# Kernel optimization log

Measured on AMD Instinct MI355X. Metric: run time of the kernel, lower is better.

Reference implementation:

```python
import jax, jax.numpy as jnp
import numpy as np

REG_MAX = 16  # number of DFL bins per box side
N = 1_048_576  # number of box predictions


def setup_inputs() -> dict:
    key = jax.random.key(0)
    k1, k2, k3 = jax.random.split(key, 3)
    pred = jax.random.normal(k1, (N, 4 * REG_MAX), dtype=jnp.float32)
    # targets are continuous bin coordinates in [0, reg_max - 1]
    target = jax.random.uniform(k2, (N, 4), dtype=jnp.float32, minval=0.0, maxval=REG_MAX - 1)
    weight = jax.random.uniform(k3, (N, 1), dtype=jnp.float32)
    return {"pred": pred, "target": target, "weight": weight}


def _target_distribution(target):
    # two-hot soft label: mass split between floor(t) and floor(t)+1 bins
    t = jnp.clip(target, 0.0, REG_MAX - 1)              # [N,4]
    left = jnp.floor(t).astype(jnp.int32)               # [N,4]
    right = jnp.clip(left + 1, 0, REG_MAX - 1)          # [N,4]
    w_right = t - left.astype(t.dtype)
    w_left = 1.0 - w_right
    oh_left = jax.nn.one_hot(left, REG_MAX, dtype=t.dtype)   # [N,4,REG_MAX]
    oh_right = jax.nn.one_hot(right, REG_MAX, dtype=t.dtype)
    return oh_left * w_left[..., None] + oh_right * w_right[..., None]


def reference(pred, target, weight):
    p = pred.reshape(-1, 4, REG_MAX)                     # [N,4,REG_MAX]
    td = _target_distribution(target.reshape(-1, 4))     # [N,4,REG_MAX]
    logp = jax.nn.log_softmax(p, axis=-1)
    # KL-div pointwise: td * (log(td) - logp), with 0 where td == 0 (xlogy semantics)
    safe_log_td = jnp.log(jnp.where(td > 0, td, 1.0))
    kl = jnp.where(td > 0, td * (safe_log_td - logp), 0.0).sum(axis=-1)  # [N,4]
    loss = kl * weight                                    # weight broadcasts [N,1] -> [N,4]
    return loss.mean()
```

## Files before the change

### kernel.cpp

```cpp
#include <hip/hip_runtime.h>

#define REG_MAX 16
#define NROWS   1048576
#define NTASK   (NROWS * 4)
#define NBLOCKS 2048
#define NTHREADS 256

__device__ __forceinline__ float dfl_task(const float* __restrict__ pred,
                                          const float* __restrict__ target,
                                          const float* __restrict__ weight,
                                          int task, int q)
{
    const float4 v = *reinterpret_cast<const float4*>(
        pred + (size_t)task * REG_MAX + q * 4);

    float s = __expf(v.x) + __expf(v.y) + __expf(v.z) + __expf(v.w);
    s += __shfl_xor(s, 1);
    s += __shfl_xor(s, 2);
    const float lse = __logf(s);

    float t = target[task];
    t = fminf(fmaxf(t, 0.0f), 15.0f);
    const float lf = floorf(t);
    const int   li = (int)lf;
    const int   ri = min(li + 1, REG_MAX - 1);
    const float wr = t - lf;
    const float wl = 1.0f - wr;

    float kl = 0.0f;
    const int base = q * 4;

    {
        const int il = li - base;
        if (il >= 0 && il < 4) {
            float pv = v.x;
            pv = (il == 1) ? v.y : pv;
            pv = (il == 2) ? v.z : pv;
            pv = (il == 3) ? v.w : pv;
            kl += wl * (__logf(wl) - (pv - lse));
        }
    }
    if (wr > 0.0f) {
        const int ir = ri - base;
        if (ir >= 0 && ir < 4) {
            float pv = v.x;
            pv = (ir == 1) ? v.y : pv;
            pv = (ir == 2) ? v.z : pv;
            pv = (ir == 3) ? v.w : pv;
            kl += wr * (__logf(wr) - (pv - lse));
        }
    }
    return kl * weight[task >> 2];
}

__global__ __launch_bounds__(NTHREADS) void dfl_partial_kernel(
    const float* __restrict__ pred,
    const float* __restrict__ target,
    const float* __restrict__ weight,
    float* __restrict__ partials)
{
    __shared__ float sm[NTHREADS / 64];
    const int gid     = blockIdx.x * NTHREADS + threadIdx.x;
    const int group   = gid >> 2;
    const int q       = gid & 3;
    const int ngroups = (gridDim.x * NTHREADS) >> 2;

    float acc = 0.0f;
    for (int task = group; task < NTASK; task += 2 * ngroups) {
        acc += dfl_task(pred, target, weight, task, q);
        acc += dfl_task(pred, target, weight, task + ngroups, q);
    }

    for (int off = 32; off > 0; off >>= 1) acc += __shfl_down(acc, off);
    const int lane = threadIdx.x & 63;
    const int wv   = threadIdx.x >> 6;
    if (lane == 0) sm[wv] = acc;
    __syncthreads();
    if (threadIdx.x == 0)
        partials[blockIdx.x] = sm[0] + sm[1] + sm[2] + sm[3];
}

__global__ __launch_bounds__(NTHREADS) void dfl_final_kernel(
    const float* __restrict__ partials, int n, float* __restrict__ out)
{
    __shared__ float sm[NTHREADS / 64];
    float acc = 0.0f;
    for (int i = threadIdx.x; i < n; i += NTHREADS) acc += partials[i];
    for (int off = 32; off > 0; off >>= 1) acc += __shfl_down(acc, off);
    const int lane = threadIdx.x & 63;
    const int wv   = threadIdx.x >> 6;
    if (lane == 0) sm[wv] = acc;
    __syncthreads();
    if (threadIdx.x == 0)
        out[0] = (sm[0] + sm[1] + sm[2] + sm[3]) * (1.0f / (float)NTASK);
}

extern "C" void kernel_launch(void* const* d_in, const int* in_sizes, int n_in,
                              void* d_out, int out_size, void* d_ws, size_t ws_size,
                              hipStream_t stream) {
    const float* pred   = (const float*)d_in[0];
    const float* target = (const float*)d_in[1];
    const float* weight = (const float*)d_in[2];
    float* out      = (float*)d_out;
    float* partials = (float*)d_ws;

    dfl_partial_kernel<<<NBLOCKS, NTHREADS, 0, stream>>>(pred, target, weight, partials);
    dfl_final_kernel<<<1, NTHREADS, 0, stream>>>(partials, NBLOCKS, out);
}
```

Measured before the change: 55.34 us.

## Process one DFL task per thread with tent-weight dot product instead of lane shuffles

Each thread now loads all 16 logits of a box side (four 16-byte loads) instead of four lanes sharing one side through xor shuffles. The KL term is rewritten as entropy + logsumexp - dot(target_dist, logits), with the two-hot distribution expressed as a branch-free tent weight max(1-|t-i|,0). This removes the shuffles and the select chains, but each thread's memory access becomes strided by 64 bytes and it holds 16 values in registers. The logsumexp still has no max subtraction, as before.

Result: faster. 52.66 us (-4.8%).

```diff
diff --git a/kernel.cpp b/kernel.cpp
--- a/kernel.cpp
+++ b/kernel.cpp
@@ -1,56 +1,60 @@
 #include <hip/hip_runtime.h>
 
-#define REG_MAX 16
-#define NROWS   1048576
-#define NTASK   (NROWS * 4)
-#define NBLOCKS 2048
+#define REG_MAX  16
+#define NROWS    1048576
+#define NTASK    (NROWS * 4)
+#define NBLOCKS  2048
 #define NTHREADS 256
+#define NTOTAL   (NBLOCKS * NTHREADS)
+
+typedef float f32x4 __attribute__((ext_vector_type(4)));
 
 __device__ __forceinline__ float dfl_task(const float* __restrict__ pred,
                                           const float* __restrict__ target,
                                           const float* __restrict__ weight,
-                                          int task, int q)
+                                          int task)
 {
-    const float4 v = *reinterpret_cast<const float4*>(
-        pred + (size_t)task * REG_MAX + q * 4);
-
-    float s = __expf(v.x) + __expf(v.y) + __expf(v.z) + __expf(v.w);
-    s += __shfl_xor(s, 1);
-    s += __shfl_xor(s, 2);
-    const float lse = __logf(s);
+    const f32x4* p = reinterpret_cast<const f32x4*>(pred + (size_t)task * REG_MAX);
+    const f32x4 a = p[0], b = p[1], c = p[2], d = p[3];
 
     float t = target[task];
     t = fminf(fmaxf(t, 0.0f), 15.0f);
+
+    float s0, s1, s2, s3;
+    float d0, d1, d2, d3;
+
+#define BIN0(v, i)  { s0  = __expf(v); float cf = fmaxf(1.0f - fabsf(t - (float)(i)), 0.0f); d0  = cf * (v); }
+#define BIN(v, i, sk, dk) { sk += __expf(v); float cf = fmaxf(1.0f - fabsf(t - (float)(i)), 0.0f); dk = fmaf(cf, (v), dk); }
+
+    BIN0(a.x, 0)
+    s1 = __expf(a.y); { float cf = fmaxf(1.0f - fabsf(t - 1.0f), 0.0f); d1 = cf * a.y; }
+    s2 = __expf(a.z); { float cf = fmaxf(1.0f - fabsf(t - 2.0f), 0.0f); d2 = cf * a.z; }
+    s3 = __expf(a.w); { float cf = fmaxf(1.0f - fabsf(t - 3.0f), 0.0f); d3 = cf * a.w; }
+    BIN(b.x,  4, s0, d0)
+    BIN(b.y,  5, s1, d1)
+    BIN(b.z,  6, s2, d2)
+    BIN(b.w,  7, s3, d3)
+    BIN(c.x,  8, s0, d0)
+    BIN(c.y,  9, s1, d1)
+    BIN(c.z, 10, s2, d2)
+    BIN(c.w, 11, s3, d3)
+    BIN(d.x, 12, s0, d0)
+    BIN(d.y, 13, s1, d1)
+    BIN(d.z, 14, s2, d2)
+    BIN(d.w, 15, s3, d3)
+#undef BIN0
+#undef BIN
+
+    const float s   = (s0 + s1) + (s2 + s3);
+    const float dot = (d0 + d1) + (d2 + d3);
+    const float lse = __logf(s);
+
     const float lf = floorf(t);
-    const int   li = (int)lf;
-    const int   ri = min(li + 1, REG_MAX - 1);
     const float wr = t - lf;
     const float wl = 1.0f - wr;
+    const float h = wl * __logf(wl) + wr * __logf(fmaxf(wr, 1e-30f));
 
-    float kl = 0.0f;
-    const int base = q * 4;
-
-    {
-        const int il = li - base;
-        if (il >= 0 && il < 4) {
-            float pv = v.x;
-            pv = (il == 1) ? v.y : pv;
-            pv = (il == 2) ? v.z : pv;
-            pv = (il == 3) ? v.w : pv;
-            kl += wl * (__logf(wl) - (pv - lse));
-        }
-    }
-    if (wr > 0.0f) {
-        const int ir = ri - base;
-        if (ir >= 0 && ir < 4) {
-            float pv = v.x;
-            pv = (ir == 1) ? v.y : pv;
-            pv = (ir == 2) ? v.z : pv;
-            pv = (ir == 3) ? v.w : pv;
-            kl += wr * (__logf(wr) - (pv - lse));
-        }
-    }
-    return kl * weight[task >> 2];
+    return (h + lse - dot) * weight[task >> 2];
 }
 
 __global__ __launch_bounds__(NTHREADS) void dfl_partial_kernel(
@@ -60,15 +64,12 @@
     float* __restrict__ partials)
 {
     __shared__ float sm[NTHREADS / 64];
-    const int gid     = blockIdx.x * NTHREADS + threadIdx.x;
-    const int group   = gid >> 2;
-    const int q       = gid & 3;
-    const int ngroups = (gridDim.x * NTHREADS) >> 2;
+    const int tid = blockIdx.x * NTHREADS + threadIdx.x;
 
     float acc = 0.0f;
-    for (int task = group; task < NTASK; task += 2 * ngroups) {
-        acc += dfl_task(pred, target, weight, task, q);
-        acc += dfl_task(pred, target, weight, task + ngroups, q);
+    for (int task = tid; task < NTASK; task += 2 * NTOTAL) {
+        acc += dfl_task(pred, target, weight, task);
+        acc += dfl_task(pred, target, weight, task + NTOTAL);
     }
 
     for (int off = 32; off > 0; off >>= 1) acc += __shfl_down(acc, off);
```
